# Performance work log

Hardware: AMD Instinct MI355X
Metric: run time of the kernel (lower is better)

Reference implementation:

```python
import jax, jax.numpy as jnp
import numpy as np

IN_DIM = 256
QK_DIM = IN_DIM // 8


def setup_inputs() -> dict:
    key = jax.random.key(0)
    ks = jax.random.split(key, 7)
    B, C, H, W = 4, IN_DIM, 64, 64
    s = 0.05
    return {
        "x": jax.random.normal(ks[0], (B, C, H, W), dtype=jnp.float32),
        "Wq": jax.random.normal(ks[1], (QK_DIM, C), dtype=jnp.float32) * s,
        "bq": jnp.zeros((QK_DIM,), dtype=jnp.float32),
        "Wk": jax.random.normal(ks[2], (QK_DIM, C), dtype=jnp.float32) * s,
        "bk": jnp.zeros((QK_DIM,), dtype=jnp.float32),
        "Wv": jax.random.normal(ks[3], (C, C), dtype=jnp.float32) * s,
        "bv": jnp.zeros((C,), dtype=jnp.float32),
        "gamma": jnp.zeros((1,), dtype=jnp.float32),
    }


def reference(x, Wq, bq, Wk, bk, Wv, bv, gamma):
    B, C, H, W = x.shape
    N = H * W
    xf = x.reshape(B, C, N)  # [B, C, N]
    # 1x1 convs are channel matmuls
    q = jnp.einsum('oc,bcn->bno', Wq, xf) + bq  # [B, N, Cqk]
    k = jnp.einsum('oc,bcn->bon', Wk, xf) + bk[None, :, None]  # [B, Cqk, N]
    energy = jnp.einsum('bno,bom->bnm', q, k)  # [B, N, N]
    attn = jax.nn.softmax(energy, axis=-1)
    v = jnp.einsum('oc,bcn->bon', Wv, xf) + bv[None, :, None]  # [B, C, N]
    # torch: out = bmm(v, attn^T) -> out[b,c,m] = sum_n v[b,c,n]*attn[m,n]
    out = jnp.einsum('bcn,bmn->bcm', v, attn)
    out = out.reshape(B, C, H, W)
    return gamma[0] * out + x
```

## Files before the change

### kernel.cpp

```cpp
#include <hip/hip_runtime.h>
#include <hip/hip_bf16.h>
#include <cstddef>

#define NB  4
#define NC  256
#define NN  4096
#define DQK 32
#define MT  64
#define JT  64
#define NIT (NN / JT)
#define XSTR 40
#define LOG2E 1.44269504088896340736f

typedef __attribute__((ext_vector_type(8))) short short8;
typedef __attribute__((ext_vector_type(4))) float f32x4;

#define MFMA16(a, b, c) __builtin_amdgcn_mfma_f32_16x16x32_bf16((a), (b), (c), 0, 0, 0)

__device__ inline unsigned pk2bf(float a, float b) {
  __hip_bfloat162 h = __float22bfloat162_rn(make_float2(a, b));
  unsigned u;
  __builtin_memcpy(&u, &h, 4);
  return u;
}

__device__ inline void bar_lgkm() {
  asm volatile("s_waitcnt lgkmcnt(0)" ::: "memory");
  __builtin_amdgcn_s_barrier();
}

__global__ __launch_bounds__(256) void wcvt_kernel(
    const float* __restrict__ Wq, const float* __restrict__ Wk,
    const float* __restrict__ Wv, __hip_bfloat16* __restrict__ W16) {
  const int id4 = (blockIdx.x * 256 + threadIdx.x) * 4;
  const int row = id4 >> 8, col = id4 & 255;
  const float* src = (row < 32) ? Wq + row * 256
                   : (row < 64) ? Wk + (row - 32) * 256
                                : Wv + (row - 64) * 256;
  float4 vv = *(const float4*)(src + col);
  if (row < 32) { vv.x *= LOG2E; vv.y *= LOG2E; vv.z *= LOG2E; vv.w *= LOG2E; }
  *(uint2*)(W16 + id4) = make_uint2(pk2bf(vv.x, vv.y), pk2bf(vv.z, vv.w));
}

__global__ __launch_bounds__(256) void proj_kernel(
    const float* __restrict__ x, const __hip_bfloat16* __restrict__ W16,
    const float* __restrict__ bq, const float* __restrict__ bk,
    const float* __restrict__ bv, __hip_bfloat16* __restrict__ q,
    __hip_bfloat16* __restrict__ kT, __hip_bfloat16* __restrict__ v) {
  __shared__ __hip_bfloat16 Xs[32 * XSTR];
  const int t = threadIdx.x;
  const int b = blockIdx.y, n0 = blockIdx.x * 32;
  const int w = __builtin_amdgcn_readfirstlane(t >> 6);
  const int ln = t & 15, quad = (t & 63) >> 4;
  const int sn = t & 31, scg = t >> 5;

  f32x4 zero4 = {0.f, 0.f, 0.f, 0.f};
  f32x4 acc[5][2];
#pragma unroll
  for (int i = 0; i < 5; ++i)
#pragma unroll
    for (int j = 0; j < 2; ++j) acc[i][j] = zero4;

  const float* xsrc = x + (size_t)b * NC * NN + n0 + sn;
  float xr[4];
#pragma unroll
  for (int i = 0; i < 4; ++i) xr[i] = xsrc[(size_t)(scg * 4 + i) * NN];

  short8 afc[5];
#pragma unroll
  for (int ot = 0; ot < 5; ++ot)
    afc[ot] = *(const short8*)(W16 + (size_t)(w * 80 + ot * 16 + ln) * NC + quad * 8);

  for (int k0 = 0; k0 < NC; k0 += 32) {
    const unsigned px0 = pk2bf(xr[0], xr[1]);
    const unsigned px1 = pk2bf(xr[2], xr[3]);
    bar_lgkm();
    *(uint2*)&Xs[sn * XSTR + scg * 4] = make_uint2(px0, px1);
    const int kn = (k0 + 32) & (NC - 1);
#pragma unroll
    for (int i = 0; i < 4; ++i) xr[i] = xsrc[(size_t)(kn + scg * 4 + i) * NN];
    short8 afn[5];
#pragma unroll
    for (int ot = 0; ot < 5; ++ot)
      afn[ot] = *(const short8*)(W16 + (size_t)(w * 80 + ot * 16 + ln) * NC + kn + quad * 8);
    bar_lgkm();
    short8 bfr[2];
#pragma unroll
    for (int nt = 0; nt < 2; ++nt)
      bfr[nt] = *(const short8*)&Xs[(nt * 16 + ln) * XSTR + quad * 8];
#pragma unroll
    for (int ot = 0; ot < 5; ++ot)
#pragma unroll
      for (int nt = 0; nt < 2; ++nt)
        acc[ot][nt] = MFMA16(afc[ot], bfr[nt], acc[ot][nt]);
#pragma unroll
    for (int ot = 0; ot < 5; ++ot) afc[ot] = afn[ot];
  }

#pragma unroll
  for (int ot = 0; ot < 5; ++ot) {
    const int gbase = w * 80 + ot * 16;
    if (gbase < 32) {
#pragma unroll
      for (int nt = 0; nt < 2; ++nt)
#pragma unroll
        for (int r = 0; r < 4; ++r) {
          const int row = gbase + quad * 4 + r;
          q[((size_t)b * NN + n0 + nt * 16 + ln) * DQK + row] =
              __hip_bfloat16(acc[ot][nt][r] + bq[row] * LOG2E);
        }
    } else if (gbase < 64) {
#pragma unroll
      for (int nt = 0; nt < 2; ++nt)
#pragma unroll
        for (int r = 0; r < 4; ++r) {
          const int row = gbase - 32 + quad * 4 + r;
          kT[((size_t)b * NN + n0 + nt * 16 + ln) * DQK + row] =
              __hip_bfloat16(acc[ot][nt][r] + bk[row]);
        }
    } else {
#pragma unroll
      for (int nt = 0; nt < 2; ++nt)
#pragma unroll
        for (int r = 0; r < 4; ++r) {
          const int c = gbase - 64 + quad * 4 + r;
          v[((size_t)b * NC + c) * NN + n0 + nt * 16 + ln] =
              __hip_bfloat16(acc[ot][nt][r] + bv[c]);
        }
    }
  }
}

__global__ __launch_bounds__(512, 2) void flash_kernel(
    const __hip_bfloat16* __restrict__ q, const __hip_bfloat16* __restrict__ kt,
    const __hip_bfloat16* __restrict__ v, const float* __restrict__ x,
    const float* __restrict__ gamma, float* __restrict__ out) {
  __shared__ __align__(16) __hip_bfloat16 Ps[2][MT * 64];
  __shared__ float lrow[MT];

  const int t  = threadIdx.x;
  const int bi = blockIdx.x;
  const int b  = (bi & 7) >> 1;
  const int m0 = (((bi & 1) * 32) + (bi >> 3)) * MT;

  const int w    = __builtin_amdgcn_readfirstlane(t >> 6);
  const int ln   = t & 15;
  const int quad = (t & 63) >> 4;

  const __hip_bfloat16* kb_base = kt + (size_t)b * NN * DQK;
  const __hip_bfloat16* v_base  = v + (size_t)b * NC * NN;

  if (w < 4) {
    const short8 qa =
        *(const short8*)(q + ((size_t)b * NN + m0 + w * 16 + ln) * DQK + quad * 8);
    float lreg[4] = {0.f, 0.f, 0.f, 0.f};
    const f32x4 zero4 = {0.f, 0.f, 0.f, 0.f};
    short8 kb[4];
#pragma unroll
    for (int jt = 0; jt < 4; ++jt)
      kb[jt] = *(const short8*)(kb_base + (size_t)(jt * 16 + ln) * DQK + quad * 8);

    for (int it = 0; it < NIT; ++it) {
      f32x4 sf[4];
#pragma unroll
      for (int jt = 0; jt < 4; ++jt) sf[jt] = MFMA16(qa, kb[jt], zero4);

      if (it + 1 < NIT) {
        const int jn = (it + 1) * JT;
#pragma unroll
        for (int jt = 0; jt < 4; ++jt)
          kb[jt] = *(const short8*)(kb_base + (size_t)(jn + jt * 16 + ln) * DQK + quad * 8);
      }

      char* pbase = (char*)&Ps[it & 1][0];
#pragma unroll
      for (int jt = 0; jt < 4; ++jt)
#pragma unroll
        for (int r = 0; r < 4; ++r) {
          const int m = w * 16 + quad * 4 + r;
          const float e = exp2f(sf[jt][r]);
          lreg[r] += e;
          *(__hip_bfloat16*)(pbase + m * 128 +
                             ((2 * (jt * 16 + ln)) ^ ((m & 7) << 4))) = __hip_bfloat16(e);
        }
      bar_lgkm();
    }
#pragma unroll
    for (int off = 1; off < 16; off <<= 1)
#pragma unroll
      for (int r = 0; r < 4; ++r) lreg[r] += __shfl_xor(lreg[r], off);
    if (ln == 0) {
#pragma unroll
      for (int r = 0; r < 4; ++r) lrow[w * 16 + quad * 4 + r] = lreg[r];
    }
    bar_lgkm();
  } else {
    const int c0 = (w - 4) * 64;
    const f32x4 zero4 = {0.f, 0.f, 0.f, 0.f};
    f32x4 acc[4][4];
#pragma unroll
    for (int ct = 0; ct < 4; ++ct)
#pragma unroll
      for (int mt = 0; mt < 4; ++mt) acc[ct][mt] = zero4;

    short8 va[4][2];
#pragma unroll
    for (int ct = 0; ct < 4; ++ct)
#pragma unroll
      for (int ks = 0; ks < 2; ++ks)
        va[ct][ks] = *(const short8*)(v_base +
            (size_t)(c0 + ct * 16 + ln) * NN + ks * 32 + quad * 8);
    bar_lgkm();

    for (int it = 1; it < NIT; ++it) {
      const char* pbase = (const char*)&Ps[(it - 1) & 1][0];
#pragma unroll
      for (int ks = 0; ks < 2; ++ks) {
        short8 pb[4];
#pragma unroll
        for (int mt = 0; mt < 4; ++mt)
          pb[mt] = *(const short8*)(pbase + (mt * 16 + ln) * 128 +
                                    ((ks * 64 + quad * 16) ^ ((ln & 7) << 4)));
#pragma unroll
        for (int ct = 0; ct < 4; ++ct)
#pragma unroll
          for (int mt = 0; mt < 4; ++mt)
            acc[ct][mt] = MFMA16(va[ct][ks], pb[mt], acc[ct][mt]);
      }

      const int j0 = it * JT;
#pragma unroll
      for (int ct = 0; ct < 4; ++ct)
#pragma unroll
        for (int ks = 0; ks < 2; ++ks)
          va[ct][ks] = *(const short8*)(v_base +
              (size_t)(c0 + ct * 16 + ln) * NN + j0 + ks * 32 + quad * 8);
      bar_lgkm();
    }

    {
      const char* pbase = (const char*)&Ps[(NIT - 1) & 1][0];
#pragma unroll
      for (int ks = 0; ks < 2; ++ks) {
        short8 pb[4];
#pragma unroll
        for (int mt = 0; mt < 4; ++mt)
          pb[mt] = *(const short8*)(pbase + (mt * 16 + ln) * 128 +
                                    ((ks * 64 + quad * 16) ^ ((ln & 7) << 4)));
#pragma unroll
        for (int ct = 0; ct < 4; ++ct)
#pragma unroll
          for (int mt = 0; mt < 4; ++mt)
            acc[ct][mt] = MFMA16(va[ct][ks], pb[mt], acc[ct][mt]);
      }
    }
    bar_lgkm();

    const float g0 = gamma[0];
    float li[4];
#pragma unroll
    for (int mt = 0; mt < 4; ++mt) li[mt] = 1.f / lrow[mt * 16 + ln];
#pragma unroll
    for (int ct = 0; ct < 4; ++ct)
#pragma unroll
      for (int r = 0; r < 4; ++r) {
        const int c = c0 + ct * 16 + quad * 4 + r;
        const float* xr = x + ((size_t)b * NC + c) * NN + m0;
        float* orow = out + ((size_t)b * NC + c) * NN + m0;
#pragma unroll
        for (int mt = 0; mt < 4; ++mt) {
          const int m = mt * 16 + ln;
          orow[m] = g0 * (acc[ct][mt][r] * li[mt]) + xr[m];
        }
      }
  }
}

extern "C" void kernel_launch(void* const* d_in, const int* in_sizes, int n_in,
                              void* d_out, int out_size, void* d_ws, size_t ws_size,
                              hipStream_t stream) {
  const float* x     = (const float*)d_in[0];
  const float* Wq    = (const float*)d_in[1];
  const float* bq    = (const float*)d_in[2];
  const float* Wk    = (const float*)d_in[3];
  const float* bk    = (const float*)d_in[4];
  const float* Wv    = (const float*)d_in[5];
  const float* bv    = (const float*)d_in[6];
  const float* gamma = (const float*)d_in[7];
  float* out = (float*)d_out;

  char* wsp = (char*)d_ws;
  __hip_bfloat16* W16 = (__hip_bfloat16*)wsp;  wsp += (size_t)320 * NC * 2;
  __hip_bfloat16* q   = (__hip_bfloat16*)wsp;  wsp += (size_t)NB * NN * DQK * 2;
  __hip_bfloat16* kT  = (__hip_bfloat16*)wsp;  wsp += (size_t)NB * NN * DQK * 2;
  __hip_bfloat16* v   = (__hip_bfloat16*)wsp;

  wcvt_kernel<<<dim3(80), dim3(256), 0, stream>>>(Wq, Wk, Wv, W16);
  proj_kernel<<<dim3(NN / 32, NB), dim3(256), 0, stream>>>(x, W16, bq, bk, bv, q, kT, v);
  flash_kernel<<<dim3(NB * NN / MT), dim3(512), 0, stream>>>(q, kT, v, x, gamma, out);
}
```

Measured before the change: 170.5 us.

## Double flash key tile, transpose score MFMA, preload full X slab in projection

```diff
diff --git a/kernel.cpp b/kernel.cpp
--- a/kernel.cpp
+++ b/kernel.cpp
@@ -7,9 +7,9 @@
 #define NN  4096
 #define DQK 32
 #define MT  64
-#define JT  64
+#define JT  128
 #define NIT (NN / JT)
-#define XSTR 40
+#define XS2 264
 #define LOG2E 1.44269504088896340736f
 
 typedef __attribute__((ext_vector_type(8))) short short8;
@@ -47,13 +47,31 @@
     const float* __restrict__ bq, const float* __restrict__ bk,
     const float* __restrict__ bv, __hip_bfloat16* __restrict__ q,
     __hip_bfloat16* __restrict__ kT, __hip_bfloat16* __restrict__ v) {
-  __shared__ __hip_bfloat16 Xs[32 * XSTR];
+  __shared__ __hip_bfloat16 Xs[32 * XS2];
   const int t = threadIdx.x;
   const int b = blockIdx.y, n0 = blockIdx.x * 32;
   const int w = __builtin_amdgcn_readfirstlane(t >> 6);
   const int ln = t & 15, quad = (t & 63) >> 4;
   const int sn = t & 31, scg = t >> 5;
 
+  const float* xsrc = x + (size_t)b * NC * NN + n0 + sn;
+  float xr[4][8];
+#pragma unroll
+  for (int g = 0; g < 4; ++g)
+#pragma unroll
+    for (int i = 0; i < 8; ++i)
+      xr[g][i] = xsrc[(size_t)(g * 64 + scg * 8 + i) * NN];
+#pragma unroll
+  for (int g = 0; g < 4; ++g) {
+    uint4 pw;
+    pw.x = pk2bf(xr[g][0], xr[g][1]);
+    pw.y = pk2bf(xr[g][2], xr[g][3]);
+    pw.z = pk2bf(xr[g][4], xr[g][5]);
+    pw.w = pk2bf(xr[g][6], xr[g][7]);
+    *(uint4*)&Xs[sn * XS2 + g * 64 + scg * 8] = pw;
+  }
+  bar_lgkm();
+
   f32x4 zero4 = {0.f, 0.f, 0.f, 0.f};
   f32x4 acc[5][2];
 #pragma unroll
@@ -61,40 +79,20 @@
 #pragma unroll
     for (int j = 0; j < 2; ++j) acc[i][j] = zero4;
 
-  const float* xsrc = x + (size_t)b * NC * NN + n0 + sn;
-  float xr[4];
-#pragma unroll
-  for (int i = 0; i < 4; ++i) xr[i] = xsrc[(size_t)(scg * 4 + i) * NN];
-
-  short8 afc[5];
-#pragma unroll
-  for (int ot = 0; ot < 5; ++ot)
-    afc[ot] = *(const short8*)(W16 + (size_t)(w * 80 + ot * 16 + ln) * NC + quad * 8);
-
+#pragma unroll
   for (int k0 = 0; k0 < NC; k0 += 32) {
-    const unsigned px0 = pk2bf(xr[0], xr[1]);
-    const unsigned px1 = pk2bf(xr[2], xr[3]);
-    bar_lgkm();
-    *(uint2*)&Xs[sn * XSTR + scg * 4] = make_uint2(px0, px1);
-    const int kn = (k0 + 32) & (NC - 1);
-#pragma unroll
-    for (int i = 0; i < 4; ++i) xr[i] = xsrc[(size_t)(kn + scg * 4 + i) * NN];
-    short8 afn[5];
+    short8 af[5], bfr[2];
 #pragma unroll
     for (int ot = 0; ot < 5; ++ot)
-      afn[ot] = *(const short8*)(W16 + (size_t)(w * 80 + ot * 16 + ln) * NC + kn + quad * 8);
-    bar_lgkm();
-    short8 bfr[2];
+      af[ot] = *(const short8*)(W16 + (size_t)(w * 80 + ot * 16 + ln) * NC + k0 + quad * 8);
 #pragma unroll
     for (int nt = 0; nt < 2; ++nt)
-      bfr[nt] = *(const short8*)&Xs[(nt * 16 + ln) * XSTR + quad * 8];
+      bfr[nt] = *(const short8*)&Xs[(nt * 16 + ln) * XS2 + k0 + quad * 8];
 #pragma unroll
     for (int ot = 0; ot < 5; ++ot)
 #pragma unroll
       for (int nt = 0; nt < 2; ++nt)
-        acc[ot][nt] = MFMA16(afc[ot], bfr[nt], acc[ot][nt]);
-#pragma unroll
-    for (int ot = 0; ot < 5; ++ot) afc[ot] = afn[ot];
+        acc[ot][nt] = MFMA16(af[ot], bfr[nt], acc[ot][nt]);
   }
 
 #pragma unroll
@@ -135,7 +133,7 @@
     const __hip_bfloat16* __restrict__ q, const __hip_bfloat16* __restrict__ kt,
     const __hip_bfloat16* __restrict__ v, const float* __restrict__ x,
     const float* __restrict__ gamma, float* __restrict__ out) {
-  __shared__ __align__(16) __hip_bfloat16 Ps[2][MT * 64];
+  __shared__ __align__(16) __hip_bfloat16 Ps[2][MT * JT];
   __shared__ float lrow[MT];
 
   const int t  = threadIdx.x;
@@ -153,46 +151,44 @@
   if (w < 4) {
     const short8 qa =
         *(const short8*)(q + ((size_t)b * NN + m0 + w * 16 + ln) * DQK + quad * 8);
-    float lreg[4] = {0.f, 0.f, 0.f, 0.f};
+    float lreg = 0.f;
     const f32x4 zero4 = {0.f, 0.f, 0.f, 0.f};
-    short8 kb[4];
-#pragma unroll
-    for (int jt = 0; jt < 4; ++jt)
+    short8 kb[8];
+#pragma unroll
+    for (int jt = 0; jt < 8; ++jt)
       kb[jt] = *(const short8*)(kb_base + (size_t)(jt * 16 + ln) * DQK + quad * 8);
 
+    const int m  = w * 16 + ln;
+    char* prow_swz0 = nullptr;
+
     for (int it = 0; it < NIT; ++it) {
-      f32x4 sf[4];
-#pragma unroll
-      for (int jt = 0; jt < 4; ++jt) sf[jt] = MFMA16(qa, kb[jt], zero4);
+      f32x4 st[8];
+      __builtin_amdgcn_s_setprio(1);
+#pragma unroll
+      for (int jt = 0; jt < 8; ++jt) st[jt] = MFMA16(kb[jt], qa, zero4);
+      __builtin_amdgcn_s_setprio(0);
 
       if (it + 1 < NIT) {
         const int jn = (it + 1) * JT;
 #pragma unroll
-        for (int jt = 0; jt < 4; ++jt)
+        for (int jt = 0; jt < 8; ++jt)
           kb[jt] = *(const short8*)(kb_base + (size_t)(jn + jt * 16 + ln) * DQK + quad * 8);
       }
 
-      char* pbase = (char*)&Ps[it & 1][0];
-#pragma unroll
-      for (int jt = 0; jt < 4; ++jt)
-#pragma unroll
-        for (int r = 0; r < 4; ++r) {
-          const int m = w * 16 + quad * 4 + r;
-          const float e = exp2f(sf[jt][r]);
-          lreg[r] += e;
-          *(__hip_bfloat16*)(pbase + m * 128 +
-                             ((2 * (jt * 16 + ln)) ^ ((m & 7) << 4))) = __hip_bfloat16(e);
-        }
+      char* pbase = (char*)&Ps[it & 1][0] + m * (JT * 2);
+#pragma unroll
+      for (int jt = 0; jt < 8; ++jt) {
+        const float e0 = exp2f(st[jt][0]), e1 = exp2f(st[jt][1]);
+        const float e2 = exp2f(st[jt][2]), e3 = exp2f(st[jt][3]);
+        lreg += (e0 + e1) + (e2 + e3);
+        *(uint2*)(pbase + ((jt * 32 + quad * 8) ^ ((m & 7) << 4))) =
+            make_uint2(pk2bf(e0, e1), pk2bf(e2, e3));
+      }
       bar_lgkm();
     }
-#pragma unroll
-    for (int off = 1; off < 16; off <<= 1)
-#pragma unroll
-      for (int r = 0; r < 4; ++r) lreg[r] += __shfl_xor(lreg[r], off);
-    if (ln == 0) {
-#pragma unroll
-      for (int r = 0; r < 4; ++r) lrow[w * 16 + quad * 4 + r] = lreg[r];
-    }
+    lreg += __shfl_xor(lreg, 16);
+    lreg += __shfl_xor(lreg, 32);
+    if (quad == 0) lrow[w * 16 + ln] = lreg;
     bar_lgkm();
   } else {
     const int c0 = (w - 4) * 64;
@@ -203,55 +199,56 @@
 #pragma unroll
       for (int mt = 0; mt < 4; ++mt) acc[ct][mt] = zero4;
 
-    short8 va[4][2];
+    short8 va[4][4];
 #pragma unroll
     for (int ct = 0; ct < 4; ++ct)
 #pragma unroll
-      for (int ks = 0; ks < 2; ++ks)
+      for (int ks = 0; ks < 4; ++ks)
         va[ct][ks] = *(const short8*)(v_base +
             (size_t)(c0 + ct * 16 + ln) * NN + ks * 32 + quad * 8);
     bar_lgkm();
 
     for (int it = 1; it < NIT; ++it) {
       const char* pbase = (const char*)&Ps[(it - 1) & 1][0];
-#pragma unroll
-      for (int ks = 0; ks < 2; ++ks) {
+      const int j0 = it * JT;
+#pragma unroll
+      for (int ks = 0; ks < 4; ++ks) {
         short8 pb[4];
 #pragma unroll
         for (int mt = 0; mt < 4; ++mt)
-          pb[mt] = *(const short8*)(pbase + (mt * 16 + ln) * 128 +
+          pb[mt] = *(const short8*)(pbase + (mt * 16 + ln) * (JT * 2) +
                                     ((ks * 64 + quad * 16) ^ ((ln & 7) << 4)));
+        __builtin_amdgcn_s_setprio(1);
 #pragma unroll
         for (int ct = 0; ct < 4; ++ct)
 #pragma unroll
           for (int mt = 0; mt < 4; ++mt)
             acc[ct][mt] = MFMA16(va[ct][ks], pb[mt], acc[ct][mt]);
-      }
-
-      const int j0 = it * JT;
-#pragma unroll
-      for (int ct = 0; ct < 4; ++ct)
-#pragma unroll
-        for (int ks = 0; ks < 2; ++ks)
+        __builtin_amdgcn_s_setprio(0);
+#pragma unroll
+        for (int ct = 0; ct < 4; ++ct)
           va[ct][ks] = *(const short8*)(v_base +
               (size_t)(c0 + ct * 16 + ln) * NN + j0 + ks * 32 + quad * 8);
+      }
       bar_lgkm();
     }
 
     {
       const char* pbase = (const char*)&Ps[(NIT - 1) & 1][0];
 #pragma unroll
-      for (int ks = 0; ks < 2; ++ks) {
+      for (int ks = 0; ks < 4; ++ks) {
         short8 pb[4];
 #pragma unroll
         for (int mt = 0; mt < 4; ++mt)
-          pb[mt] = *(const short8*)(pbase + (mt * 16 + ln) * 128 +
+          pb[mt] = *(const short8*)(pbase + (mt * 16 + ln) * (JT * 2) +
                                     ((ks * 64 + quad * 16) ^ ((ln & 7) << 4)));
+        __builtin_amdgcn_s_setprio(1);
 #pragma unroll
         for (int ct = 0; ct < 4; ++ct)
 #pragma unroll
           for (int mt = 0; mt < 4; ++mt)
             acc[ct][mt] = MFMA16(va[ct][ks], pb[mt], acc[ct][mt]);
+        __builtin_amdgcn_s_setprio(0);
       }
     }
     bar_lgkm();
```

Measured after the change: 171.3 us. No clear change (+0.5%).
